# Kernel tuning notes

Measured on AMD Instinct MI355X. Metric: run time of the kernel, lower is better.

The kernel has to match this reference:

```python
import jax, jax.numpy as jnp
import numpy as np

B, T, C = 4, 2048, 1024
H = 16
D = C // H  # head_dim = 64


def setup_inputs() -> dict:
    key = jax.random.key(0)
    k1, k2, k3, k4, k5 = jax.random.split(key, 5)
    s = 1.0 / np.sqrt(C)
    return {
        "x": jax.random.normal(k1, (B, T, C), dtype=jnp.float32),
        "Wqkv": jax.random.normal(k2, (C, 3 * C), dtype=jnp.float32) * s,
        "bqkv": jax.random.normal(k3, (3 * C,), dtype=jnp.float32) * 0.02,
        "Wproj": jax.random.normal(k4, (C, C), dtype=jnp.float32) * s,
        "bproj": jax.random.normal(k5, (C,), dtype=jnp.float32) * 0.02,
    }


def reference(x, Wqkv, bqkv, Wproj, bproj):
    b, t, c = x.shape
    qkv = x @ Wqkv + bqkv                      # [B,T,3C]
    qkv = qkv.reshape(b, t, 3, H, D)
    q, k, v = (qkv[:, :, i].transpose(0, 2, 1, 3) for i in range(3))  # [B,H,T,D]
    scale = D ** -0.5
    attn = jnp.einsum("bhqd,bhkd->bhqk", q, k) * scale
    causal = jnp.tril(jnp.ones((t, t), dtype=bool))
    attn = jnp.where(causal[None, None], attn, -jnp.inf)
    attn = jax.nn.softmax(attn, axis=-1)
    out = jnp.einsum("bhqk,bhkd->bhqd", attn, v)  # [B,H,T,D]
    out = out.transpose(0, 2, 1, 3).reshape(b, t, c)
    return out @ Wproj + bproj
```

## Files before the change

### kernel.cpp

```cpp
#include <hip/hip_runtime.h>
#include <hip/hip_bf16.h>

typedef __bf16 bf16;
typedef __bf16 bf16x4 __attribute__((ext_vector_type(4)));
typedef __bf16 bf16x8 __attribute__((ext_vector_type(8)));
typedef float  f32x4  __attribute__((ext_vector_type(4)));

#define DEV static __device__ __forceinline__

static constexpr int Bsz = 4, T = 2048, C = 1024, H = 16;
static constexpr int M  = Bsz * T;
static constexpr int N1 = 3 * C;
static constexpr float SM_SCALE = 0.125f;

DEV void gload16(const bf16* g, const bf16* l) {
  __builtin_amdgcn_global_load_lds(
      (const __attribute__((address_space(1))) void*)g,
      (__attribute__((address_space(3))) void*)l, 16, 0, 0);
}

__launch_bounds__(256)
__global__ void convert_kernel(const float* __restrict__ in, bf16* __restrict__ out) {
  const size_t i = ((size_t)blockIdx.x * 256 + threadIdx.x) * 8;
  f32x4 a = *(const f32x4*)(in + i);
  f32x4 b = *(const f32x4*)(in + i + 4);
  *(bf16x4*)(out + i)     = __builtin_convertvector(a, bf16x4);
  *(bf16x4*)(out + i + 4) = __builtin_convertvector(b, bf16x4);
}

__launch_bounds__(256)
__global__ void transpose_conv_kernel(const float* __restrict__ in,
                                      bf16* __restrict__ out, int K, int N) {
  __shared__ float t[32][33];
  const int n0 = blockIdx.x * 32, k0 = blockIdx.y * 32;
  const int tx = threadIdx.x & 31, ty = threadIdx.x >> 5;
#pragma unroll
  for (int j = 0; j < 4; ++j)
    t[ty + j * 8][tx] = in[(size_t)(k0 + ty + j * 8) * N + n0 + tx];
  __syncthreads();
#pragma unroll
  for (int j = 0; j < 4; ++j)
    out[(size_t)(n0 + ty + j * 8) * K + k0 + tx] = (bf16)t[tx][ty + j * 8];
}

template <bool OUT_BF16, bool V_SPLIT>
__launch_bounds__(256)
__global__ void gemm_kernel(const bf16* __restrict__ A,
                            const bf16* __restrict__ Bt,
                            const float* __restrict__ bias,
                            void* __restrict__ Out, bf16* __restrict__ vt,
                            int Ndim, int Kdim) {
  __shared__ bf16 lds_a[128 * 64];
  __shared__ bf16 lds_b[128 * 64];
  const int tid = threadIdx.x;
  const int l = tid & 63, wid = tid >> 6;
  const int wm = wid >> 1, wn = wid & 1;
  const int lr = l & 15, lh = l >> 4;
  const int m0 = blockIdx.x * 128, n0 = blockIdx.y * 128;
  const int r8 = l >> 3, g8 = (l & 7) * 8;

  f32x4 acc[4][4] = {};

  for (int k0 = 0; k0 < Kdim; k0 += 64) {
    __syncthreads();
#pragma unroll
    for (int i = 0; i < 4; ++i) {
      const int c = wid * 4 + i;
      const int row = c * 8 + r8;
      gload16(A  + (size_t)(m0 + row) * Kdim + k0 + g8, &lds_a[c * 512]);
      gload16(Bt + (size_t)(n0 + row) * Kdim + k0 + g8, &lds_b[c * 512]);
    }
    __syncthreads();
#pragma unroll
    for (int kk = 0; kk < 2; ++kk) {
      bf16x8 af[4], bfr[4];
#pragma unroll
      for (int mi = 0; mi < 4; ++mi)
        af[mi] = *(const bf16x8*)&lds_a[(wm * 64 + mi * 16 + lr) * 64 + kk * 32 + lh * 8];
#pragma unroll
      for (int ni = 0; ni < 4; ++ni)
        bfr[ni] = *(const bf16x8*)&lds_b[(wn * 64 + ni * 16 + lr) * 64 + kk * 32 + lh * 8];
#pragma unroll
      for (int mi = 0; mi < 4; ++mi)
#pragma unroll
        for (int ni = 0; ni < 4; ++ni)
          acc[mi][ni] = __builtin_amdgcn_mfma_f32_16x16x32_bf16(
              af[mi], bfr[ni], acc[mi][ni], 0, 0, 0);
    }
  }
  if (V_SPLIT && n0 >= 2 * C) {
    const int b = m0 >> 11, tb = (m0 & 2047) + wm * 64;
#pragma unroll
    for (int ni = 0; ni < 4; ++ni) {
      const int col = n0 - 2 * C + wn * 64 + ni * 16 + lr;
      const int hh = col >> 6, dd = col & 63;
      const float bv = bias[2 * C + col];
      bf16* vdst = vt + ((size_t)((b * H + hh) * 64 + dd)) * T + tb + lh * 4;
#pragma unroll
      for (int mi = 0; mi < 4; ++mi) {
        bf16x4 p4;
#pragma unroll
        for (int r = 0; r < 4; ++r) p4[r] = (bf16)(acc[mi][ni][r] + bv);
        *(bf16x4*)&vdst[mi * 16] = p4;
      }
    }
  } else {
#pragma unroll
    for (int ni = 0; ni < 4; ++ni) {
      const int col = n0 + wn * 64 + ni * 16 + lr;
      const float bv = bias[col];
#pragma unroll
      for (int mi = 0; mi < 4; ++mi) {
#pragma unroll
        for (int r = 0; r < 4; ++r) {
          const int row = m0 + wm * 64 + mi * 16 + lh * 4 + r;
          const float v = acc[mi][ni][r] + bv;
          if (OUT_BF16)
            ((bf16*)Out)[(size_t)row * Ndim + col] = (bf16)v;
          else
            ((float*)Out)[(size_t)row * Ndim + col] = v;
        }
      }
    }
  }
}

DEV int vswz3(int d) { return (d & 7) ^ ((d >> 3) & 7); }

__launch_bounds__(512, 4)
__global__ void attn_kernel(const bf16* __restrict__ qk,
                            const bf16* __restrict__ vt,
                            bf16* __restrict__ out) {
  __shared__ bf16 lds_k[2][128 * 64];
  __shared__ bf16 lds_vt[2][64 * 128];
  __shared__ bf16 lds_p[8][16 * 64];
  const int tid = threadIdx.x, l = tid & 63, w = tid >> 6;
  const int lr = l & 15, lh = l >> 4;
  const int p = blockIdx.x;
  const int bh = p >> 3, jj = p & 7;
  const int b = bh >> 4, h = bh & 15;
  const size_t RS = 2 * C;
  const bf16* base  = qk + (size_t)b * T * RS;
  const bf16* kbase = base + C + h * 64;
  const bf16* vth   = vt + (size_t)bh * 64 * T;
  bf16* op = out + (size_t)b * T * C + h * 64;
  const int r1 = tid >> 3, cc = tid & 7;
  const int kc = cc ^ (r1 & 7);
  const int dV = tid >> 4, cV = tid & 15;

  auto STAGE = [&](int nb, int kt) {
#pragma unroll
    for (int i = 0; i < 2; ++i) {
      const int rowK = i * 64 + r1;
      gload16(kbase + (size_t)(kt * 128 + rowK) * RS + kc * 8,
              &lds_k[nb][i * 4096 + w * 512]);
      const int d = i * 32 + dV;
      const int vc = (cV & 8) | (((cV & 7) ^ vswz3(d)) & 7);
      gload16(vth + (size_t)d * T + kt * 128 + vc * 8,
              &lds_vt[nb][i * 4096 + w * 512]);
    }
  };

  for (int it = 0; it < 2; ++it) {
    const int J = it ? jj : 15 - jj;
    const int q16 = J * 128 + w * 16;
    bf16x8 qf[2];
#pragma unroll
    for (int kk = 0; kk < 2; ++kk) {
      bf16x8 qv = *(const bf16x8*)(base + (size_t)(q16 + lr) * RS + h * 64 + kk * 32 + lh * 8);
#pragma unroll
      for (int j = 0; j < 8; ++j) qf[kk][j] = (bf16)((float)qv[j] * SM_SCALE);
    }

    float mq = -__builtin_inff(), lq = 0.f;
    f32x4 o[4] = {};

    __syncthreads();
    STAGE(0, 0);
    __syncthreads();

    int buf = 0;
    for (int kt = 0; kt <= J; ++kt) {
      const bf16* kb = &lds_k[buf][0];
      const bf16* vb = &lds_vt[buf][0];
      if (kt < J) STAGE(buf ^ 1, kt + 1);

      f32x4 s8[8] = {};
      __builtin_amdgcn_s_setprio(1);
#pragma unroll
      for (int kk = 0; kk < 2; ++kk) {
#pragma unroll
        for (int kn = 0; kn < 8; ++kn) {
          const int key = kn * 16 + lr;
          bf16x8 kf = *(const bf16x8*)&kb[(key * 64 + kk * 32 + lh * 8) ^ ((key & 7) << 3)];
          s8[kn] = __builtin_amdgcn_mfma_f32_16x16x32_bf16(kf, qf[kk], s8[kn], 0, 0, 0);
        }
      }
      __builtin_amdgcn_s_setprio(0);
      if (kt == J) {
        const int qloc = w * 16 + lr;
#pragma unroll
        for (int kn = 0; kn < 8; ++kn)
#pragma unroll
          for (int r = 0; r < 4; ++r)
            if ((kn * 16 + lh * 4 + r) > qloc) s8[kn][r] = -__builtin_inff();
      }
      float pm = s8[0][0];
#pragma unroll
      for (int kn = 0; kn < 8; ++kn)
#pragma unroll
        for (int r = 0; r < 4; ++r) pm = fmaxf(pm, s8[kn][r]);
      pm = fmaxf(pm, __shfl_xor(pm, 16));
      pm = fmaxf(pm, __shfl_xor(pm, 32));
      const float mnew = fmaxf(mq, pm);
      const float alpha_q = __expf(mq - mnew);
      mq = mnew;
      float ssum = 0.f;
#pragma unroll
      for (int kn = 0; kn < 8; ++kn)
#pragma unroll
        for (int r = 0; r < 4; ++r) {
          const float p2 = __expf(s8[kn][r] - mnew);
          s8[kn][r] = p2;
          ssum += p2;
        }
      ssum += __shfl_xor(ssum, 16);
      ssum += __shfl_xor(ssum, 32);
      lq = lq * alpha_q + ssum;
      float al[4];
#pragma unroll
      for (int r = 0; r < 4; ++r) al[r] = __shfl(alpha_q, lh * 4 + r);
#pragma unroll
      for (int ni = 0; ni < 4; ++ni)
#pragma unroll
        for (int r = 0; r < 4; ++r) o[ni][r] *= al[r];
#pragma unroll
      for (int hh = 0; hh < 2; ++hh) {
#pragma unroll
        for (int kn4 = 0; kn4 < 4; ++kn4) {
          const int kn = hh * 4 + kn4;
          bf16x4 pb;
#pragma unroll
          for (int r = 0; r < 4; ++r) pb[r] = (bf16)s8[kn][r];
          *(bf16x4*)&lds_p[w][(lr * 64 + kn4 * 16 + lh * 4) ^ ((lr & 7) << 3)] = pb;
        }
        __builtin_amdgcn_s_setprio(1);
#pragma unroll
        for (int kkl = 0; kkl < 2; ++kkl) {
          bf16x8 pf = *(const bf16x8*)&lds_p[w][(lr * 64 + kkl * 32 + lh * 8) ^ ((lr & 7) << 3)];
#pragma unroll
          for (int ni = 0; ni < 4; ++ni) {
            const int d = ni * 16 + lr;
            const int key = hh * 64 + kkl * 32 + lh * 8;
            bf16x8 vf = *(const bf16x8*)&vb[d * 128 + (key ^ (vswz3(d) << 3))];
            o[ni] = __builtin_amdgcn_mfma_f32_16x16x32_bf16(pf, vf, o[ni], 0, 0, 0);
          }
        }
        __builtin_amdgcn_s_setprio(0);
      }

      if (kt < J) {
        __syncthreads();
        buf ^= 1;
      }
    }
    float lrec[4];
#pragma unroll
    for (int r = 0; r < 4; ++r) lrec[r] = 1.0f / __shfl(lq, lh * 4 + r);
#pragma unroll
    for (int ni = 0; ni < 4; ++ni)
#pragma unroll
      for (int r = 0; r < 4; ++r) {
        const int qrow = q16 + lh * 4 + r;
        op[(size_t)qrow * C + ni * 16 + lr] = (bf16)(o[ni][r] * lrec[r]);
      }
  }
}

extern "C" void kernel_launch(void* const* d_in, const int* in_sizes, int n_in,
                              void* d_out, int out_size, void* d_ws, size_t ws_size,
                              hipStream_t stream) {
  const float* x     = (const float*)d_in[0];
  const float* Wqkv  = (const float*)d_in[1];
  const float* bqkv  = (const float*)d_in[2];
  const float* Wproj = (const float*)d_in[3];
  const float* bproj = (const float*)d_in[4];
  float* out = (float*)d_out;

  char* ws = (char*)d_ws;
  bf16* qk       = (bf16*)(ws);
  bf16* vt       = (bf16*)(ws + 33554432);
  bf16* wqkvt    = (bf16*)(ws + 50331648);
  bf16* wprojt   = (bf16*)(ws + 56623104);
  bf16* attn_out = (bf16*)(ws + 58720256);
  bf16* x_bf16   = attn_out;

  convert_kernel<<<dim3(M * C / (256 * 8)), 256, 0, stream>>>(x, x_bf16);
  transpose_conv_kernel<<<dim3(N1 / 32, C / 32), 256, 0, stream>>>(Wqkv, wqkvt, C, N1);
  transpose_conv_kernel<<<dim3(C / 32, C / 32), 256, 0, stream>>>(Wproj, wprojt, C, C);
  gemm_kernel<true, true><<<dim3(M / 128, N1 / 128), 256, 0, stream>>>(
      x_bf16, wqkvt, bqkv, qk, vt, 2 * C, C);
  attn_kernel<<<dim3(Bsz * H * 8), 512, 0, stream>>>(qk, vt, attn_out);
  gemm_kernel<false, false><<<dim3(M / 128, C / 128), 256, 0, stream>>>(
      attn_out, wprojt, bproj, out, nullptr, C, C);
}
```

Measured before the change: 291.9 us.

## Rewrite GEMM with 128x256 tiles, 8 waves, triple-buffered swizzled LDS pipeline

Replaces the 128x128 single-buffered GEMM with a 512-thread 128x256 tile kernel that prefetches K-tiles two steps ahead into three LDS buffers, with explicit vmcnt waits and barriers. LDS rows are XOR-swizzled to avoid bank conflicts on fragment reads, and MFMA sections are raised in priority. The goal is to hide global-load latency and the double sync per K step. In exchange it uses much more LDS (144KB) and forces one block per CU, and the grid shrinks, which may hurt occupancy and wave balance on the smaller projection GEMM.

```diff
diff --git a/kernel.cpp b/kernel.cpp
--- a/kernel.cpp
+++ b/kernel.cpp
@@ -44,50 +44,93 @@
 }
 
 template <bool OUT_BF16, bool V_SPLIT>
-__launch_bounds__(256)
-__global__ void gemm_kernel(const bf16* __restrict__ A,
-                            const bf16* __restrict__ Bt,
-                            const float* __restrict__ bias,
-                            void* __restrict__ Out, bf16* __restrict__ vt,
-                            int Ndim, int Kdim) {
-  __shared__ bf16 lds_a[128 * 64];
-  __shared__ bf16 lds_b[128 * 64];
-  const int tid = threadIdx.x;
-  const int l = tid & 63, wid = tid >> 6;
-  const int wm = wid >> 1, wn = wid & 1;
+__launch_bounds__(512, 1)
+__global__ void gemm8_kernel(const bf16* __restrict__ A,
+                             const bf16* __restrict__ Bt,
+                             const float* __restrict__ bias,
+                             void* __restrict__ Out, bf16* __restrict__ vt,
+                             int Ndim, int Kdim) {
+  __shared__ bf16 ldsA[3][128 * 64];
+  __shared__ bf16 ldsB[3][256 * 64];
+  const int tid = threadIdx.x, l = tid & 63, w = tid >> 6;
+  const int wm = w >> 2, wn = w & 3;
   const int lr = l & 15, lh = l >> 4;
-  const int m0 = blockIdx.x * 128, n0 = blockIdx.y * 128;
-  const int r8 = l >> 3, g8 = (l & 7) * 8;
+  const int m0 = blockIdx.x * 128, n0 = blockIdx.y * 256;
+  const int rA = tid >> 3, cA = tid & 7;
+  const int cs = cA ^ (rA & 7);
+
+  auto STAGE = [&](int nb, int t) {
+    const int k0 = t * 64;
+#pragma unroll
+    for (int i = 0; i < 2; ++i) {
+      const int row = i * 64 + rA;
+      gload16(A + (size_t)(m0 + row) * Kdim + k0 + cs * 8,
+              &ldsA[nb][i * 4096 + w * 512]);
+    }
+#pragma unroll
+    for (int i = 0; i < 4; ++i) {
+      const int row = i * 64 + rA;
+      gload16(Bt + (size_t)(n0 + row) * Kdim + k0 + cs * 8,
+              &ldsB[nb][i * 4096 + w * 512]);
+    }
+  };
 
   f32x4 acc[4][4] = {};
-
-  for (int k0 = 0; k0 < Kdim; k0 += 64) {
-    __syncthreads();
-#pragma unroll
-    for (int i = 0; i < 4; ++i) {
-      const int c = wid * 4 + i;
-      const int row = c * 8 + r8;
-      gload16(A  + (size_t)(m0 + row) * Kdim + k0 + g8, &lds_a[c * 512]);
-      gload16(Bt + (size_t)(n0 + row) * Kdim + k0 + g8, &lds_b[c * 512]);
-    }
-    __syncthreads();
+  const int NT = Kdim >> 6;
+
+  STAGE(0, 0);
+  STAGE(1, 1);
+  asm volatile("s_waitcnt vmcnt(6)" ::: "memory");
+  __builtin_amdgcn_sched_barrier(0);
+  __builtin_amdgcn_s_barrier();
+  __builtin_amdgcn_sched_barrier(0);
+
+  for (int t = 0; t < NT; ++t) {
+    const int cur = t % 3;
+    const bool more = (t + 2) < NT;
+    if (more) STAGE((t + 2) % 3, t + 2);
+    __builtin_amdgcn_sched_barrier(0);
+
+    const bf16* a_ = &ldsA[cur][0];
+    const bf16* b_ = &ldsB[cur][0];
+    bf16x8 af[2][4], bfm[2][4];
 #pragma unroll
     for (int kk = 0; kk < 2; ++kk) {
-      bf16x8 af[4], bfr[4];
-#pragma unroll
-      for (int mi = 0; mi < 4; ++mi)
-        af[mi] = *(const bf16x8*)&lds_a[(wm * 64 + mi * 16 + lr) * 64 + kk * 32 + lh * 8];
-#pragma unroll
-      for (int ni = 0; ni < 4; ++ni)
-        bfr[ni] = *(const bf16x8*)&lds_b[(wn * 64 + ni * 16 + lr) * 64 + kk * 32 + lh * 8];
+#pragma unroll
+      for (int mi = 0; mi < 4; ++mi) {
+        const int row = wm * 64 + mi * 16 + lr;
+        af[kk][mi] = *(const bf16x8*)&a_[row * 64 + (((kk * 4 + lh) ^ (row & 7)) << 3)];
+      }
+#pragma unroll
+      for (int ni = 0; ni < 4; ++ni) {
+        const int row = wn * 64 + ni * 16 + lr;
+        bfm[kk][ni] = *(const bf16x8*)&b_[row * 64 + (((kk * 4 + lh) ^ (row & 7)) << 3)];
+      }
+    }
+    __builtin_amdgcn_s_setprio(1);
+#pragma unroll
+    for (int kk = 0; kk < 2; ++kk)
 #pragma unroll
       for (int mi = 0; mi < 4; ++mi)
 #pragma unroll
         for (int ni = 0; ni < 4; ++ni)
           acc[mi][ni] = __builtin_amdgcn_mfma_f32_16x16x32_bf16(
-              af[mi], bfr[ni], acc[mi][ni], 0, 0, 0);
+              af[kk][mi], bfm[kk][ni], acc[mi][ni], 0, 0, 0);
+    __builtin_amdgcn_s_setprio(0);
+    __builtin_amdgcn_sched_barrier(0);
+
+    if (t + 1 < NT) {
+      if (more) {
+        asm volatile("s_waitcnt vmcnt(6)" ::: "memory");
+      } else {
+        asm volatile("s_waitcnt vmcnt(0)" ::: "memory");
+      }
+      __builtin_amdgcn_sched_barrier(0);
+      __builtin_amdgcn_s_barrier();
+      __builtin_amdgcn_sched_barrier(0);
     }
   }
+
   if (V_SPLIT && n0 >= 2 * C) {
     const int b = m0 >> 11, tb = (m0 & 2047) + wm * 64;
 #pragma unroll
@@ -298,9 +341,9 @@
   convert_kernel<<<dim3(M * C / (256 * 8)), 256, 0, stream>>>(x, x_bf16);
   transpose_conv_kernel<<<dim3(N1 / 32, C / 32), 256, 0, stream>>>(Wqkv, wqkvt, C, N1);
   transpose_conv_kernel<<<dim3(C / 32, C / 32), 256, 0, stream>>>(Wproj, wprojt, C, C);
-  gemm_kernel<true, true><<<dim3(M / 128, N1 / 128), 256, 0, stream>>>(
+  gemm8_kernel<true, true><<<dim3(M / 128, N1 / 256), 512, 0, stream>>>(
       x_bf16, wqkvt, bqkv, qk, vt, 2 * C, C);
   attn_kernel<<<dim3(Bsz * H * 8), 512, 0, stream>>>(qk, vt, attn_out);
-  gemm_kernel<false, false><<<dim3(M / 128, C / 128), 256, 0, stream>>>(
+  gemm8_kernel<false, false><<<dim3(M / 128, C / 256), 512, 0, stream>>>(
       attn_out, wprojt, bproj, out, nullptr, C, C);
 }
```

After: 283.7 us. -2.8%, faster.
